# Performance work log

Hardware: AMD Instinct MI355X
Metric: run time of the kernel (lower is better)

The kernel has to match this reference:

```python
import jax, jax.numpy as jnp
import numpy as np
from jax import lax

ALPHA = 0.3          # opt['retrieval_strategy']['margin']
NB_SAMPLES = 10      # hardest negatives kept per anchor
W_IRR = 1.0
W_RII = 1.0
B = 4096
D = 1024
NB_CLASSES = 1048


def _pairwise_dist(x, y):
    # Euclidean pairwise distance matrix [B, B] (self.dist in the torch module)
    x2 = jnp.sum(x * x, axis=1, keepdims=True)          # [B,1]
    y2 = jnp.sum(y * y, axis=1, keepdims=True).T        # [1,B]
    d2 = x2 + y2 - 2.0 * (x @ y.T)
    return jnp.sqrt(jnp.maximum(d2, 0.0))


def setup_inputs() -> dict:
    key = jax.random.key(0)
    k1, k2, k3, k4 = jax.random.split(key, 4)
    input1 = jax.random.normal(k1, (B, D), dtype=jnp.float32)
    input2 = jax.random.normal(k2, (B, D), dtype=jnp.float32)
    # target==1 everywhere -> 'matches' mask selects the whole batch (identity gather)
    target = jnp.ones((B, 1), dtype=jnp.int32)
    # classes in [1, NB_CLASSES) -> all rows valid (class != 0)
    class1 = jax.random.randint(k3, (B, 1), 1, NB_CLASSES, dtype=jnp.int32)
    class2 = jax.random.randint(k4, (B, 1), 1, NB_CLASSES, dtype=jnp.int32)
    return {"input1": input1, "input2": input2, "target": target,
            "class1": class1, "class2": class2}


def _mine(cost):
    # calculate_cost with sampling='max_negative': sort rows descending, keep nb_samples.
    # top_k == descending sort truncated to k.
    top, _ = lax.top_k(cost, NB_SAMPLES)                # [B, NB_SAMPLES]
    return top


def reference(input1, input2, target, class1, class2):
    # matches = (target == 1) is all-true by construction -> instance_* = full inputs
    dist = _pairwise_dist(input1, input2)               # [B, B]
    diag = jnp.diagonal(dist)                           # [B]
    n = dist.shape[0]
    eye = jnp.eye(n, dtype=bool)

    # IRR: anchor image, positive its own recipe, negatives other recipes
    cost_irr = jnp.maximum(diag[:, None] - dist + ALPHA, 0.0)
    cost_irr = jnp.where(eye, 0.0, cost_irr)
    top_irr = _mine(cost_irr)
    bad_irr = jnp.mean((top_irr == 0.0).astype(jnp.float32))
    loss_irr = top_irr.mean() * W_IRR

    # RII: anchor recipe, positive its own image, negatives other images (cost.t())
    cost_rii = jnp.maximum(diag[None, :] - dist + ALPHA, 0.0)
    cost_rii = jnp.where(eye, 0.0, cost_rii)
    top_rii = _mine(cost_rii.T)
    bad_rii = jnp.mean((top_rii == 0.0).astype(jnp.float32))
    loss_rii = top_rii.mean() * W_RII

    return jnp.stack([loss_irr, loss_rii, bad_irr, bad_rii])
```

## Files before the change

kernel.cpp:

```cpp
#include <hip/hip_runtime.h>
#include <hip/hip_fp16.h>

#define ALPHA 0.3f
#define B_SZ 4096
#define D_SZ 1024
#define CT_STRIDE 132
#define BIGF 3.0e38f
#define SENT_F 60000.0f

typedef __attribute__((ext_vector_type(8))) _Float16 half8;
typedef __attribute__((ext_vector_type(4))) _Float16 half4;
typedef __attribute__((ext_vector_type(2))) _Float16 half2v;
typedef __attribute__((ext_vector_type(4))) float floatx4;

typedef __attribute__((address_space(1))) const void* gas_t;
typedef __attribute__((address_space(3))) void* las_t;

__device__ __forceinline__ float wave_reduce_add(float v) {
#pragma unroll
    for (int off = 32; off; off >>= 1) v += __shfl_xor(v, off);
    return v;
}

__device__ __forceinline__ void insert10(float (&best)[10], float x) {
#pragma unroll
    for (int p = 0; p < 10; ++p) {
        float lo = fminf(best[p], x);
        x = fmaxf(best[p], x);
        best[p] = lo;
    }
}

__device__ __forceinline__ void insert10p(half2v (&b)[10], half2v x) {
#pragma unroll
    for (int p = 0; p < 10; ++p) {
        half2v lo = __builtin_elementwise_min(b[p], x);
        x = __builtin_elementwise_max(b[p], x);
        b[p] = lo;
    }
}

__device__ __forceinline__ unsigned short h16(float x) {
    return __builtin_bit_cast(unsigned short, (_Float16)x);
}

__global__ void __launch_bounds__(256) prep_kernel(
    const float* __restrict__ in1, const float* __restrict__ in2,
    _Float16* __restrict__ Xh, _Float16* __restrict__ Yh,
    float* __restrict__ x2, float* __restrict__ y2, float* __restrict__ mth) {
    int row = blockIdx.x;
    int t = threadIdx.x;
    const float4* a4 = (const float4*)(in1 + (size_t)row * D_SZ);
    const float4* b4 = (const float4*)(in2 + (size_t)row * D_SZ);
    float4 a = a4[t], b = b4[t];
    half4 ha = {(_Float16)a.x, (_Float16)a.y, (_Float16)a.z, (_Float16)a.w};
    half4 hb = {(_Float16)b.x, (_Float16)b.y, (_Float16)b.z, (_Float16)b.w};
    ((half4*)(Xh + (size_t)row * D_SZ))[t] = ha;
    ((half4*)(Yh + (size_t)row * D_SZ))[t] = hb;
    float sa = a.x * a.x + a.y * a.y + a.z * a.z + a.w * a.w;
    float sb = b.x * b.x + b.y * b.y + b.z * b.z + b.w * b.w;
    float d0 = a.x - b.x, d1 = a.y - b.y, d2v = a.z - b.z, d3 = a.w - b.w;
    float sd = d0 * d0 + d1 * d1 + d2v * d2v + d3 * d3;
    sa = wave_reduce_add(sa);
    sb = wave_reduce_add(sb);
    sd = wave_reduce_add(sd);
    __shared__ float red[3][4];
    int wave = t >> 6, lane = t & 63;
    if (lane == 0) { red[0][wave] = sa; red[1][wave] = sb; red[2][wave] = sd; }
    __syncthreads();
    if (t == 0) {
        x2[row] = red[0][0] + red[0][1] + red[0][2] + red[0][3];
        y2[row] = red[1][0] + red[1][1] + red[1][2] + red[1][3];
        mth[row] = sqrtf(red[2][0] + red[2][1] + red[2][2] + red[2][3]) + ALPHA;
    }
}

__global__ void __launch_bounds__(256, 4) gemm_topk_kernel(
    const _Float16* __restrict__ Xh, const _Float16* __restrict__ Yh,
    const float* __restrict__ x2, const float* __restrict__ y2,
    _Float16* __restrict__ CandI, _Float16* __restrict__ CandR) {
    __shared__ _Float16 smem[16896];
    _Float16* As = smem;
    _Float16* Bs = smem + 4096;
    int tid = threadIdx.x;
    int wave = tid >> 6, lane = tid & 63;
    int waveR = wave >> 1, waveC = wave & 1;
    int bx = blockIdx.x, by = blockIdx.y;
    int q = lane >> 4, mrow = lane & 15;

    floatx4 acc[4][4] = {};

    int c0 = tid, c1 = 256 + tid;
    int r0 = c0 >> 2, q0 = (c0 & 3) ^ ((r0 >> 1) & 3);
    int r1 = c1 >> 2, q1 = (c1 & 3) ^ ((r1 >> 1) & 3);
    const _Float16* gA0 = Xh + (size_t)(by * 128 + r0) * D_SZ + q0 * 8;
    const _Float16* gB0 = Yh + (size_t)(bx * 128 + r0) * D_SZ + q0 * 8;
    const _Float16* gA1 = Xh + (size_t)(by * 128 + r1) * D_SZ + q1 * 8;
    const _Float16* gB1 = Yh + (size_t)(bx * 128 + r1) * D_SZ + q1 * 8;
    _Float16* la0 = &As[(wave * 64) * 8];
    _Float16* lb0 = &Bs[(wave * 64) * 8];
    _Float16* la1 = &As[(256 + wave * 64) * 8];
    _Float16* lb1 = &Bs[(256 + wave * 64) * 8];

    int aoff[4], boff[4];
#pragma unroll
    for (int mi = 0; mi < 4; ++mi) {
        int R = waveR * 64 + mi * 16 + mrow;
        aoff[mi] = R * 32 + (q ^ ((R >> 1) & 3)) * 8;
    }
#pragma unroll
    for (int ni = 0; ni < 4; ++ni) {
        int R = waveC * 64 + ni * 16 + mrow;
        boff[ni] = R * 32 + (q ^ ((R >> 1) & 3)) * 8;
    }

    for (int k0 = 0; k0 < D_SZ; k0 += 32) {
        __syncthreads();
        __builtin_amdgcn_global_load_lds((gas_t)(const void*)(gA0 + k0), (las_t)(void*)la0, 16, 0, 0);
        __builtin_amdgcn_global_load_lds((gas_t)(const void*)(gB0 + k0), (las_t)(void*)lb0, 16, 0, 0);
        __builtin_amdgcn_global_load_lds((gas_t)(const void*)(gA1 + k0), (las_t)(void*)la1, 16, 0, 0);
        __builtin_amdgcn_global_load_lds((gas_t)(const void*)(gB1 + k0), (las_t)(void*)lb1, 16, 0, 0);
        __syncthreads();
        half8 af[4], bf[4];
#pragma unroll
        for (int mi = 0; mi < 4; ++mi) af[mi] = *(const half8*)&As[aoff[mi]];
#pragma unroll
        for (int ni = 0; ni < 4; ++ni) bf[ni] = *(const half8*)&Bs[boff[ni]];
#pragma unroll
        for (int mi = 0; mi < 4; ++mi)
#pragma unroll
            for (int ni = 0; ni < 4; ++ni)
                acc[mi][ni] = __builtin_amdgcn_mfma_f32_16x16x32_f16(af[mi], bf[ni], acc[mi][ni], 0, 0, 0);
    }
    __syncthreads();

    _Float16* Ct = smem;
#pragma unroll
    for (int ni = 0; ni < 4; ++ni) {
        int lc = waveC * 64 + ni * 16 + mrow;
        float y2v = y2[bx * 128 + lc];
#pragma unroll
        for (int mi = 0; mi < 4; ++mi) {
            int lr0 = waveR * 64 + mi * 16 + q * 4;
            int gr0 = by * 128 + lr0;
            floatx4 v = acc[mi][ni];
            half4 hv = {(_Float16)(x2[gr0 + 0] + y2v - 2.0f * v[0]),
                        (_Float16)(x2[gr0 + 1] + y2v - 2.0f * v[1]),
                        (_Float16)(x2[gr0 + 2] + y2v - 2.0f * v[2]),
                        (_Float16)(x2[gr0 + 3] + y2v - 2.0f * v[3])};
            *(half4*)&Ct[lc * CT_STRIDE + lr0] = hv;
        }
    }
    __syncthreads();
    if (bx == by && tid < 128) Ct[tid * CT_STRIDE + tid] = (_Float16)SENT_F;
    __syncthreads();

    const half2v sent2 = {(_Float16)SENT_F, (_Float16)SENT_F};

    if (wave < 2) {
        int p = wave * 32 + (lane & 31);
        int chalf = lane >> 5;
        half2v b[10];
#pragma unroll
        for (int i = 0; i < 10; ++i) b[i] = sent2;
#pragma unroll 8
        for (int i = 0; i < 64; ++i) {
            int c = chalf * 64 + i;
            half2v v = *(const half2v*)&Ct[c * CT_STRIDE + 2 * p];
            insert10p(b, v);
        }
        half2v t[10];
#pragma unroll
        for (int k = 0; k < 10; ++k)
            t[k] = __builtin_bit_cast(half2v, __shfl_xor(__builtin_bit_cast(int, b[k]), 32));
#pragma unroll
        for (int k = 0; k < 10; ++k) insert10p(b, t[k]);
        if (lane < 32) {
            int grow = by * 128 + 2 * p;
            unsigned int* d0 = (unsigned int*)CandI + ((size_t)grow * 32 + bx) * 5;
            unsigned int* d1 = d0 + 32 * 5;
#pragma unroll
            for (int k = 0; k < 5; ++k) {
                unsigned int u0 = __builtin_bit_cast(unsigned int, b[2 * k]);
                unsigned int u1 = __builtin_bit_cast(unsigned int, b[2 * k + 1]);
                d0[k] = (u0 & 0xFFFFu) | (u1 << 16);
                d1[k] = (u0 >> 16) | (u1 & 0xFFFF0000u);
            }
        }
    } else {
        int c = (wave - 2) * 64 + lane;
        half2v b[10];
#pragma unroll
        for (int i = 0; i < 10; ++i) b[i] = sent2;
        const half2v* colp = (const half2v*)&Ct[c * CT_STRIDE];
#pragma unroll 8
        for (int i = 0; i < 64; ++i) insert10p(b, colp[i]);
        float bf[10];
#pragma unroll
        for (int i = 0; i < 10; ++i) bf[i] = BIGF;
#pragma unroll
        for (int k = 0; k < 10; ++k) {
            insert10(bf, (float)b[k][0]);
            insert10(bf, (float)b[k][1]);
        }
        int gcol = bx * 128 + c;
        unsigned int* d = (unsigned int*)CandR + ((size_t)gcol * 32 + by) * 5;
#pragma unroll
        for (int k = 0; k < 5; ++k)
            d[k] = (unsigned int)h16(bf[2 * k]) | ((unsigned int)h16(bf[2 * k + 1]) << 16);
    }
}

__global__ void __launch_bounds__(256) merge_kernel(
    const _Float16* __restrict__ CandI, const _Float16* __restrict__ CandR,
    const float* __restrict__ mth,
    float* __restrict__ Srow, float* __restrict__ Zrow) {
    int wave = threadIdx.x >> 6, lane = threadIdx.x & 63;
    int r = blockIdx.x * 4 + wave;
    int row = r & (B_SZ - 1);
    const _Float16* cp = ((r < B_SZ) ? CandI : CandR) + (size_t)row * 320;
    float best[10];
#pragma unroll
    for (int i = 0; i < 10; ++i) best[i] = BIGF;
#pragma unroll
    for (int j = 0; j < 5; ++j) insert10(best, (float)cp[j * 64 + lane]);

    float mrow = mth[row];
    float s = 0.f, z = 0.f;
#pragma unroll
    for (int round = 0; round < 10; ++round) {
        float v0 = best[0];
        float g = v0;
#pragma unroll
        for (int off = 32; off; off >>= 1) g = fminf(g, __shfl_xor(g, off));
        unsigned long long ball = __ballot(v0 == g);
        int leader = __ffsll(ball) - 1;
        if (lane == leader) {
#pragma unroll
            for (int p = 0; p < 9; ++p) best[p] = best[p + 1];
            best[9] = BIGF;
        }
        float d = sqrtf(fmaxf(g, 0.f));
        float c = fmaxf(mrow - d, 0.f);
        s += c;
        z += (c == 0.f) ? 1.f : 0.f;
    }
    if (lane == 0) { Srow[r] = s; Zrow[r] = z; }
}

__global__ void __launch_bounds__(256) finalize_kernel(
    const float* __restrict__ Srow, const float* __restrict__ Zrow,
    float* __restrict__ out) {
    __shared__ float red[256][4];
    int t = threadIdx.x;
    float s0 = 0, s1 = 0, z0 = 0, z1 = 0;
#pragma unroll
    for (int k = 0; k < 8; ++k) {
        int i = k * 256 + t;
        float4 sv = ((const float4*)Srow)[i];
        float4 zv = ((const float4*)Zrow)[i];
        float ss = sv.x + sv.y + sv.z + sv.w;
        float zz = zv.x + zv.y + zv.z + zv.w;
        if (i < 1024) { s0 += ss; z0 += zz; } else { s1 += ss; z1 += zz; }
    }
    red[t][0] = s0; red[t][1] = s1; red[t][2] = z0; red[t][3] = z1;
    __syncthreads();
    for (int off = 128; off > 0; off >>= 1) {
        if (t < off) {
#pragma unroll
            for (int j = 0; j < 4; ++j) red[t][j] += red[t + off][j];
        }
        __syncthreads();
    }
    if (t == 0) {
        const float inv = 1.0f / (float)(B_SZ * 10);
        out[0] = red[0][0] * inv;
        out[1] = red[0][1] * inv;
        out[2] = red[0][2] * inv;
        out[3] = red[0][3] * inv;
    }
}

extern "C" void kernel_launch(void* const* d_in, const int* in_sizes, int n_in,
                              void* d_out, int out_size, void* d_ws, size_t ws_size,
                              hipStream_t stream) {
    const float* in1 = (const float*)d_in[0];
    const float* in2 = (const float*)d_in[1];
    float* out = (float*)d_out;

    char* ws = (char*)d_ws;
    const size_t MB = 1024 * 1024;
    _Float16* Xh = (_Float16*)(ws);
    _Float16* Yh = (_Float16*)(ws + 8 * MB);
    _Float16* CandI = (_Float16*)(ws + 16 * MB);
    _Float16* CandR = (_Float16*)(ws + 19 * MB);
    float* x2   = (float*)(ws + 22 * MB);
    float* y2   = x2 + B_SZ;
    float* mth  = y2 + B_SZ;
    float* Srow = mth + B_SZ;
    float* Zrow = Srow + 2 * B_SZ;
    const size_t needed = 22 * MB + (size_t)(3 * B_SZ + 4 * B_SZ) * sizeof(float);
    if (ws_size < needed) return;

    hipLaunchKernelGGL(prep_kernel, dim3(B_SZ), dim3(256), 0, stream,
                       in1, in2, Xh, Yh, x2, y2, mth);
    hipLaunchKernelGGL(gemm_topk_kernel, dim3(32, 32), dim3(256), 0, stream,
                       Xh, Yh, x2, y2, CandI, CandR);
    hipLaunchKernelGGL(merge_kernel, dim3(2048), dim3(256), 0, stream,
                       CandI, CandR, mth, Srow, Zrow);
    hipLaunchKernelGGL(finalize_kernel, dim3(1), dim3(256), 0, stream,
                       Srow, Zrow, out);
}
```

Baseline: 147.0 us.

## Fold finalize into merge via atomics and merge packed-half top-10 lanes

Removes the separate finalize kernel: the prep kernel zeroes the output and each merge block reduces its partial sums and atomically adds them into the four outputs. The merge grid shrinks so each wave handles four rows. In the column top-k path, the float conversion and 20-element scalar insertion are replaced by a packed half2 swap-and-insert that combines the two halves. This trades one launch and some scalar work for atomic contention and a nondeterministic float summation order.

New measurement: 156.9 us. 6.8% more time.

```diff
diff --git a/kernel.cpp b/kernel.cpp
--- a/kernel.cpp
+++ b/kernel.cpp
@@ -40,16 +40,14 @@
     }
 }
 
-__device__ __forceinline__ unsigned short h16(float x) {
-    return __builtin_bit_cast(unsigned short, (_Float16)x);
-}
-
 __global__ void __launch_bounds__(256) prep_kernel(
     const float* __restrict__ in1, const float* __restrict__ in2,
     _Float16* __restrict__ Xh, _Float16* __restrict__ Yh,
-    float* __restrict__ x2, float* __restrict__ y2, float* __restrict__ mth) {
+    float* __restrict__ x2, float* __restrict__ y2, float* __restrict__ mth,
+    float* __restrict__ out) {
     int row = blockIdx.x;
     int t = threadIdx.x;
+    if (row == 0 && t < 4) out[t] = 0.0f;
     const float4* a4 = (const float4*)(in1 + (size_t)row * D_SZ);
     const float4* b4 = (const float4*)(in2 + (size_t)row * D_SZ);
     float4 a = a4[t], b = b4[t];
@@ -195,89 +193,71 @@
         const half2v* colp = (const half2v*)&Ct[c * CT_STRIDE];
 #pragma unroll 8
         for (int i = 0; i < 64; ++i) insert10p(b, colp[i]);
-        float bf[10];
-#pragma unroll
-        for (int i = 0; i < 10; ++i) bf[i] = BIGF;
+        half2v sw[10];
 #pragma unroll
         for (int k = 0; k < 10; ++k) {
-            insert10(bf, (float)b[k][0]);
-            insert10(bf, (float)b[k][1]);
-        }
+            unsigned int u = __builtin_bit_cast(unsigned int, b[k]);
+            sw[k] = __builtin_bit_cast(half2v, (u >> 16) | (u << 16));
+        }
+#pragma unroll
+        for (int k = 0; k < 10; ++k) insert10p(b, sw[k]);
         int gcol = bx * 128 + c;
         unsigned int* d = (unsigned int*)CandR + ((size_t)gcol * 32 + by) * 5;
 #pragma unroll
-        for (int k = 0; k < 5; ++k)
-            d[k] = (unsigned int)h16(bf[2 * k]) | ((unsigned int)h16(bf[2 * k + 1]) << 16);
+        for (int k = 0; k < 5; ++k) {
+            unsigned int u0 = __builtin_bit_cast(unsigned int, b[2 * k]);
+            unsigned int u1 = __builtin_bit_cast(unsigned int, b[2 * k + 1]);
+            d[k] = (u0 & 0xFFFFu) | (u1 << 16);
+        }
     }
 }
 
 __global__ void __launch_bounds__(256) merge_kernel(
     const _Float16* __restrict__ CandI, const _Float16* __restrict__ CandR,
-    const float* __restrict__ mth,
-    float* __restrict__ Srow, float* __restrict__ Zrow) {
+    const float* __restrict__ mth, float* __restrict__ out) {
     int wave = threadIdx.x >> 6, lane = threadIdx.x & 63;
-    int r = blockIdx.x * 4 + wave;
-    int row = r & (B_SZ - 1);
-    const _Float16* cp = ((r < B_SZ) ? CandI : CandR) + (size_t)row * 320;
-    float best[10];
-#pragma unroll
-    for (int i = 0; i < 10; ++i) best[i] = BIGF;
-#pragma unroll
-    for (int j = 0; j < 5; ++j) insert10(best, (float)cp[j * 64 + lane]);
-
-    float mrow = mth[row];
-    float s = 0.f, z = 0.f;
-#pragma unroll
-    for (int round = 0; round < 10; ++round) {
-        float v0 = best[0];
-        float g = v0;
-#pragma unroll
-        for (int off = 32; off; off >>= 1) g = fminf(g, __shfl_xor(g, off));
-        unsigned long long ball = __ballot(v0 == g);
-        int leader = __ffsll(ball) - 1;
-        if (lane == leader) {
-#pragma unroll
-            for (int p = 0; p < 9; ++p) best[p] = best[p + 1];
-            best[9] = BIGF;
-        }
-        float d = sqrtf(fmaxf(g, 0.f));
-        float c = fmaxf(mrow - d, 0.f);
-        s += c;
-        z += (c == 0.f) ? 1.f : 0.f;
-    }
-    if (lane == 0) { Srow[r] = s; Zrow[r] = z; }
-}
-
-__global__ void __launch_bounds__(256) finalize_kernel(
-    const float* __restrict__ Srow, const float* __restrict__ Zrow,
-    float* __restrict__ out) {
-    __shared__ float red[256][4];
-    int t = threadIdx.x;
-    float s0 = 0, s1 = 0, z0 = 0, z1 = 0;
-#pragma unroll
-    for (int k = 0; k < 8; ++k) {
-        int i = k * 256 + t;
-        float4 sv = ((const float4*)Srow)[i];
-        float4 zv = ((const float4*)Zrow)[i];
-        float ss = sv.x + sv.y + sv.z + sv.w;
-        float zz = zv.x + zv.y + zv.z + zv.w;
-        if (i < 1024) { s0 += ss; z0 += zz; } else { s1 += ss; z1 += zz; }
-    }
-    red[t][0] = s0; red[t][1] = s1; red[t][2] = z0; red[t][3] = z1;
-    __syncthreads();
-    for (int off = 128; off > 0; off >>= 1) {
-        if (t < off) {
-#pragma unroll
-            for (int j = 0; j < 4; ++j) red[t][j] += red[t + off][j];
-        }
-        __syncthreads();
-    }
-    if (t == 0) {
+    int side = blockIdx.x >> 8;
+    const _Float16* Cand = side ? CandR : CandI;
+    float sAcc = 0.f, zAcc = 0.f;
+#pragma unroll
+    for (int rr = 0; rr < 4; ++rr) {
+        int r = (blockIdx.x * 4 + wave) * 4 + rr;
+        int row = r & (B_SZ - 1);
+        const _Float16* cp = Cand + (size_t)row * 320;
+        float best[10];
+#pragma unroll
+        for (int i = 0; i < 10; ++i) best[i] = BIGF;
+#pragma unroll
+        for (int j = 0; j < 5; ++j) insert10(best, (float)cp[j * 64 + lane]);
+        float mrow = mth[row];
+#pragma unroll
+        for (int round = 0; round < 10; ++round) {
+            float v0 = best[0];
+            float g = v0;
+#pragma unroll
+            for (int off = 32; off; off >>= 1) g = fminf(g, __shfl_xor(g, off));
+            unsigned long long ball = __ballot(v0 == g);
+            int leader = __ffsll(ball) - 1;
+            if (lane == leader) {
+#pragma unroll
+                for (int p = 0; p < 9; ++p) best[p] = best[p + 1];
+                best[9] = BIGF;
+            }
+            float d = sqrtf(fmaxf(g, 0.f));
+            float c = fmaxf(mrow - d, 0.f);
+            sAcc += c;
+            zAcc += (c == 0.f) ? 1.f : 0.f;
+        }
+    }
+    __shared__ float red[2][4];
+    if (lane == 0) { red[0][wave] = sAcc; red[1][wave] = zAcc; }
+    __syncthreads();
+    if (threadIdx.x == 0) {
         const float inv = 1.0f / (float)(B_SZ * 10);
-        out[0] = red[0][0] * inv;
-        out[1] = red[0][1] * inv;
-        out[2] = red[0][2] * inv;
-        out[3] = red[0][3] * inv;
+        float s = (red[0][0] + red[0][1] + red[0][2] + red[0][3]) * inv;
+        float z = (red[1][0] + red[1][1] + red[1][2] + red[1][3]) * inv;
+        atomicAdd(&out[side], s);
+        atomicAdd(&out[2 + side], z);
     }
 }
 
@@ -297,17 +277,13 @@
     float* x2   = (float*)(ws + 22 * MB);
     float* y2   = x2 + B_SZ;
     float* mth  = y2 + B_SZ;
-    float* Srow = mth + B_SZ;
-    float* Zrow = Srow + 2 * B_SZ;
-    const size_t needed = 22 * MB + (size_t)(3 * B_SZ + 4 * B_SZ) * sizeof(float);
+    const size_t needed = 22 * MB + (size_t)(3 * B_SZ) * sizeof(float);
     if (ws_size < needed) return;
 
     hipLaunchKernelGGL(prep_kernel, dim3(B_SZ), dim3(256), 0, stream,
-                       in1, in2, Xh, Yh, x2, y2, mth);
+                       in1, in2, Xh, Yh, x2, y2, mth, out);
     hipLaunchKernelGGL(gemm_topk_kernel, dim3(32, 32), dim3(256), 0, stream,
                        Xh, Yh, x2, y2, CandI, CandR);
-    hipLaunchKernelGGL(merge_kernel, dim3(2048), dim3(256), 0, stream,
-                       CandI, CandR, mth, Srow, Zrow);
-    hipLaunchKernelGGL(finalize_kernel, dim3(1), dim3(256), 0, stream,
-                       Srow, Zrow, out);
-}
+    hipLaunchKernelGGL(merge_kernel, dim3(512), dim3(256), 0, stream,
+                       CandI, CandR, mth, out);
+}
```
